# Performance work log

Measured on AMD Instinct MI355X. Metric: run time of the kernel, lower is better.

## Reference

```python
import jax, jax.numpy as jnp
import numpy as np


def _conv1x1(x, w, b=None):
    # x: [B, Cin, N, S], w: [Cout, Cin], 1x1 Conv2d
    y = jnp.einsum('oc,bcns->bons', w, x)
    if b is not None:
        y = y + b[None, :, None, None]
    return y


def setup_inputs() -> dict:
    key = jax.random.key(0)
    ks = jax.random.split(key, 16)
    B, Cin, N, K = 4, 128, 16384, 16
    MID, OUT, SHARE, PT = 64, 128, 8, 10
    s = 0.05
    inp = {
        'sm_feats': jax.random.normal(ks[0], (B, Cin, N, K), jnp.float32),
        'sm_ppfs': jax.random.normal(ks[1], (B, PT, N, K), jnp.float32),
        'conv0_w': jax.random.normal(ks[2], (OUT, Cin), jnp.float32) * s,
        'conv0_b': jax.random.normal(ks[3], (OUT,), jnp.float32) * s,
        'conv1_w': jax.random.normal(ks[4], (MID, OUT), jnp.float32) * s,
        'conv1_b': jax.random.normal(ks[5], (MID,), jnp.float32) * s,
        'conv2_w': jax.random.normal(ks[6], (MID, OUT), jnp.float32) * s,
        'conv2_b': jax.random.normal(ks[7], (MID,), jnp.float32) * s,
        'conv3_w': jax.random.normal(ks[8], (MID, OUT), jnp.float32) * s,
        'conv3_b': jax.random.normal(ks[9], (MID,), jnp.float32) * s,
        'convw1_w': jax.random.normal(ks[10], (MID // SHARE, MID * K), jnp.float32) * s,
        'convw2_w': jax.random.normal(ks[11], (K * MID // SHARE, MID // SHARE), jnp.float32) * s,
        'convw2_b': jax.random.normal(ks[12], (K * MID // SHARE,), jnp.float32) * s,
        'convout_w': jax.random.normal(ks[13], (OUT, MID), jnp.float32) * s,
        'convout_b': jax.random.normal(ks[14], (OUT,), jnp.float32) * s,
        'pt1_w': jax.random.normal(ks[15], (MID, PT), jnp.float32) * s,
        'pt2_w': jax.random.normal(jax.random.fold_in(key, 99), (MID, MID), jnp.float32) * s,
    }
    return inp


def reference(sm_feats, sm_ppfs, conv0_w, conv0_b, conv1_w, conv1_b, conv2_w, conv2_b,
              conv3_w, conv3_b, convw1_w, convw2_w, convw2_b, convout_w, convout_b,
              pt1_w, pt2_w):
    xn = jax.nn.relu(_conv1x1(sm_feats, conv0_w, conv0_b))  # [B, OUT, N, K]
    x = xn[..., :1]                                          # center point feature
    identity = x
    x1 = _conv1x1(x, conv1_w, conv1_b)       # [B, MID, N, 1]
    x2 = _conv1x1(xn, conv2_w, conv2_b)      # [B, MID, N, K]
    x3 = _conv1x1(xn, conv3_w, conv3_b)      # [B, MID, N, K]
    ptf = _conv1x1(jax.nn.relu(_conv1x1(sm_ppfs, pt1_w)), pt2_w)  # [B, MID, N, K]
    x3 = x3 + ptf
    xfs = x1 - x2 + ptf                      # [B, MID, N, K]
    B, MID, N, K = xfs.shape
    share = MID // convw1_w.shape[0]
    xfs = jnp.transpose(xfs, (0, 1, 3, 2)).reshape(B, MID * K, 1, N)
    h = jax.nn.relu(_conv1x1(xfs, convw1_w))            # [B, MID//share, 1, N]
    w = _conv1x1(h, convw2_w, convw2_b)                  # [B, K*MID//share, 1, N]
    w = jax.nn.softmax(w.reshape(B, MID // share, K, N), axis=2)
    w = jnp.transpose(w, (0, 1, 3, 2))                   # [B, MID//share, N, K]
    w = jnp.tile(w, (1, share, 1, 1))                    # [B, MID, N, K]
    out = jax.nn.relu(jnp.sum(w * x3, axis=3, keepdims=True))  # [B, MID, N, 1]
    out = (_conv1x1(out, convout_w, convout_b) + identity).squeeze(3)  # [B, OUT, N]
    return out
```

## Files before the change

kernel.cpp:

```cpp
#include <hip/hip_runtime.h>
#include <hip/hip_bf16.h>


typedef __attribute__((ext_vector_type(8))) short bf16x8;
typedef __attribute__((ext_vector_type(4))) float f32x4;
typedef __attribute__((ext_vector_type(4))) unsigned short us4;

#define MFMA(a, b, c) __builtin_amdgcn_mfma_f32_16x16x32_bf16((a), (b), (c), 0, 0, 0)

#define OFF_F    0
#define OFF_X2   0
#define OFF_PTF  17408
#define OFF_XN   34816
#define OFF_X3   34816
#define OFF_XFS  52224
#define OFF_P    69632
#define OFF_WS   69632
#define OFF_HP   73984
#define OFF_HB   76032
#define OFF_OM   76288
#define OFF_X1   77824
#define OFF_XC   78848
#define SMEM_BYTES 80896

#define WS_W0  0
#define WS_W1  16384
#define WS_W2  24576
#define WS_W3  32768
#define WS_P1  40960
#define WS_P2  43008
#define WS_CW1 47104
#define WS_WO  63488
#define WS_TOTAL 71680

__device__ __forceinline__ unsigned short f2b(float f) {
    union { __hip_bfloat16 h; unsigned short u; } v;
    v.h = __float2bfloat16(f);
    return v.u;
}
__device__ __forceinline__ float b2f(unsigned short u) {
    union { unsigned u; float f; } v;
    v.u = ((unsigned)u) << 16;
    return v.f;
}
__device__ __forceinline__ us4 pk4(float a, float b, float c, float d) {
    us4 r; r[0] = f2b(a); r[1] = f2b(b); r[2] = f2b(c); r[3] = f2b(d); return r;
}
__device__ __forceinline__ bf16x8 ldb(const unsigned short* p) {
    return *(const bf16x8*)p;
}

__global__ __launch_bounds__(512, 1)
void convert_weights(const float* __restrict__ w0, const float* __restrict__ w1,
                     const float* __restrict__ w2, const float* __restrict__ w3,
                     const float* __restrict__ p1, const float* __restrict__ p2,
                     const float* __restrict__ cw1, const float* __restrict__ wo,
                     unsigned short* __restrict__ ws) {
    int i = blockIdx.x * 512 + threadIdx.x;
    if (i >= WS_TOTAL) return;
    float v;
    if (i < 16384)      v = w0[i];
    else if (i < 24576) v = w1[i - 16384];
    else if (i < 32768) v = w2[i - 24576];
    else if (i < 40960) v = w3[i - 32768];
    else if (i < 43008) { int r = i - 40960, row = r >> 5, k = r & 31;
                          v = (k < 10) ? p1[row * 10 + k] : 0.f; }
    else if (i < 47104) v = p2[i - 43008];
    else if (i < 63488) { int r = i - 47104, j = r >> 10, kc = r & 1023;
                          v = (j < 8) ? cw1[j * 1024 + (kc & 63) * 16 + (kc >> 6)] : 0.f; }
    else                v = wo[i - 63488];
    ws[i] = f2b(v);
}

__global__ __launch_bounds__(512, 4)
void fused_model_kernel(const float* __restrict__ feats, const float* __restrict__ ppfs,
                        const unsigned short* __restrict__ wsb,
                        const float* __restrict__ b0, const float* __restrict__ b1,
                        const float* __restrict__ b2, const float* __restrict__ b3,
                        const float* __restrict__ cw2, const float* __restrict__ cb2,
                        const float* __restrict__ bo, float* __restrict__ out) {
    extern __shared__ char smem[];
    const int tid = threadIdx.x;
    const int W = tid >> 6;
    const int lane = tid & 63;
    const int kk = lane & 15;
    const int g = lane >> 4;
    const int bid = blockIdx.x;
    const int b = bid >> 11;
    const int n0 = (bid & 2047) * 8;

    {
        const int kq = tid & 3, ci = tid >> 2;
        #pragma unroll
        for (int pos = 0; pos < 8; ++pos) {
            f32x4 v = *(const f32x4*)(feats + (((size_t)b * 128 + ci) * 16384 + (n0 + pos)) * 16 + kq * 4);
            char* base = smem + OFF_F + pos * 4352 + ci * 2;
            *(unsigned short*)(base + (kq * 4 + 0) * 272) = f2b(v[0]);
            *(unsigned short*)(base + (kq * 4 + 1) * 272) = f2b(v[1]);
            *(unsigned short*)(base + (kq * 4 + 2) * 272) = f2b(v[2]);
            *(unsigned short*)(base + (kq * 4 + 3) * 272) = f2b(v[3]);
        }
        if (tid < 320) {
            int pos = tid / 40, r = tid % 40, p = r >> 2, kq2 = r & 3;
            f32x4 v = *(const f32x4*)(ppfs + (((size_t)b * 10 + p) * 16384 + (n0 + pos)) * 16 + kq2 * 4);
            char* base = smem + OFF_P + pos * 1024 + p * 2;
            *(unsigned short*)(base + (kq2 * 4 + 0) * 64) = f2b(v[0]);
            *(unsigned short*)(base + (kq2 * 4 + 1) * 64) = f2b(v[1]);
            *(unsigned short*)(base + (kq2 * 4 + 2) * 64) = f2b(v[2]);
            *(unsigned short*)(base + (kq2 * 4 + 3) * 64) = f2b(v[3]);
        } else {
            for (int z = tid - 320; z < 1408; z += 192) {
                int pos = z / 176, rr = z % 176, ks = rr / 11, dw = rr % 11;
                *(unsigned*)(smem + OFF_P + pos * 1024 + ks * 64 + 20 + dw * 4) = 0u;
            }
        }
    }
    __syncthreads();

    {
        bf16x8 a0[4];
        #pragma unroll
        for (int kt = 0; kt < 4; ++kt) a0[kt] = ldb(wsb + WS_W0 + (16 * W + kk) * 128 + kt * 32 + 8 * g);
        f32x4 bv = *(const f32x4*)(b0 + 16 * W + 4 * g);
        #pragma unroll
        for (int pos = 0; pos < 8; ++pos) {
            f32x4 acc = {0.f, 0.f, 0.f, 0.f};
            #pragma unroll
            for (int kt = 0; kt < 4; ++kt) {
                bf16x8 bf = *(const bf16x8*)(smem + OFF_F + pos * 4352 + kk * 272 + (kt * 32 + 8 * g) * 2);
                acc = MFMA(a0[kt], bf, acc);
            }
            us4 xw = pk4(fmaxf(acc[0] + bv[0], 0.f), fmaxf(acc[1] + bv[1], 0.f),
                         fmaxf(acc[2] + bv[2], 0.f), fmaxf(acc[3] + bv[3], 0.f));
            *(us4*)(smem + OFF_XN + pos * 4352 + kk * 272 + (16 * W + 4 * g) * 2) = xw;
            if (kk == 0) *(us4*)(smem + OFF_XC + pos * 256 + (16 * W + 4 * g) * 2) = xw;
        }
    }
    __syncthreads();

    if (W < 4) {
        bf16x8 a1[4], a2[4][2];
        #pragma unroll
        for (int mt = 0; mt < 4; ++mt) {
            a1[mt] = ldb(wsb + WS_P1 + (16 * mt + kk) * 32 + 8 * g);
            a2[mt][0] = ldb(wsb + WS_P2 + (16 * mt + kk) * 64 + 8 * g);
            a2[mt][1] = ldb(wsb + WS_P2 + (16 * mt + kk) * 64 + 32 + 8 * g);
        }
        const int sel = g >> 1;
        const int sa = kk + 16 * ((2 * g) & 3);
        const int sb = kk + 16 * ((2 * g + 1) & 3);
        #pragma unroll
        for (int pp = 0; pp < 2; ++pp) {
            const int pos = 2 * W + pp;
            bf16x8 bp = *(const bf16x8*)(smem + OFF_P + pos * 1024 + kk * 64 + 16 * g);
            int pkd[4][2];
            #pragma unroll
            for (int mt = 0; mt < 4; ++mt) {
                f32x4 hv = {0.f, 0.f, 0.f, 0.f};
                hv = MFMA(a1[mt], bp, hv);
                us4 t = pk4(fmaxf(hv[0], 0.f), fmaxf(hv[1], 0.f),
                            fmaxf(hv[2], 0.f), fmaxf(hv[3], 0.f));
                pkd[mt][0] = ((int*)&t)[0];
                pkd[mt][1] = ((int*)&t)[1];
            }
            union { int d[4]; bf16x8 v; } bh0, bh1;
            bh0.d[0] = sel ? __shfl(pkd[1][0], sa, 64) : __shfl(pkd[0][0], sa, 64);
            bh0.d[1] = sel ? __shfl(pkd[1][1], sa, 64) : __shfl(pkd[0][1], sa, 64);
            bh0.d[2] = sel ? __shfl(pkd[1][0], sb, 64) : __shfl(pkd[0][0], sb, 64);
            bh0.d[3] = sel ? __shfl(pkd[1][1], sb, 64) : __shfl(pkd[0][1], sb, 64);
            bh1.d[0] = sel ? __shfl(pkd[3][0], sa, 64) : __shfl(pkd[2][0], sa, 64);
            bh1.d[1] = sel ? __shfl(pkd[3][1], sa, 64) : __shfl(pkd[2][1], sa, 64);
            bh1.d[2] = sel ? __shfl(pkd[3][0], sb, 64) : __shfl(pkd[2][0], sb, 64);
            bh1.d[3] = sel ? __shfl(pkd[3][1], sb, 64) : __shfl(pkd[2][1], sb, 64);
            #pragma unroll
            for (int mt = 0; mt < 4; ++mt) {
                f32x4 acc = {0.f, 0.f, 0.f, 0.f};
                acc = MFMA(a2[mt][0], bh0.v, acc);
                acc = MFMA(a2[mt][1], bh1.v, acc);
                *(us4*)(smem + OFF_PTF + pos * 2176 + kk * 136 + (16 * mt + 4 * g) * 2) =
                    pk4(acc[0], acc[1], acc[2], acc[3]);
            }
        }
    } else {
        const int mt = W - 4;
        bf16x8 aw2[4], aw1[4];
        #pragma unroll
        for (int kt = 0; kt < 4; ++kt) {
            aw2[kt] = ldb(wsb + WS_W2 + (16 * mt + kk) * 128 + kt * 32 + 8 * g);
            aw1[kt] = ldb(wsb + WS_W1 + (16 * mt + kk) * 128 + kt * 32 + 8 * g);
        }
        f32x4 b2v = *(const f32x4*)(b2 + 16 * mt + 4 * g);
        #pragma unroll
        for (int pos = 0; pos < 8; ++pos) {
            f32x4 acc = {0.f, 0.f, 0.f, 0.f};
            #pragma unroll
            for (int kt = 0; kt < 4; ++kt) {
                bf16x8 bf = *(const bf16x8*)(smem + OFF_XN + pos * 4352 + kk * 272 + (kt * 32 + 8 * g) * 2);
                acc = MFMA(aw2[kt], bf, acc);
            }
            *(us4*)(smem + OFF_X2 + pos * 2176 + kk * 136 + (16 * mt + 4 * g) * 2) =
                pk4(acc[0] + b2v[0], acc[1] + b2v[1], acc[2] + b2v[2], acc[3] + b2v[3]);
        }
        f32x4 a1c = {0.f, 0.f, 0.f, 0.f};
        #pragma unroll
        for (int kt = 0; kt < 4; ++kt) {
            bf16x8 bf = *(const bf16x8*)(smem + OFF_XN + (kk & 7) * 4352 + (kt * 32 + 8 * g) * 2);
            a1c = MFMA(aw1[kt], bf, a1c);
        }
        if (kk < 8) {
            f32x4 b1v = *(const f32x4*)(b1 + 16 * mt + 4 * g);
            *(us4*)(smem + OFF_X1 + kk * 128 + (16 * mt + 4 * g) * 2) =
                pk4(a1c[0] + b1v[0], a1c[1] + b1v[1], a1c[2] + b1v[2], a1c[3] + b1v[3]);
        }
    }
    __syncthreads();

    f32x4 acc3[4];
    {
        const int mt = W & 3, ph = W >> 2;
        bf16x8 aw3[4];
        #pragma unroll
        for (int kt = 0; kt < 4; ++kt)
            aw3[kt] = ldb(wsb + WS_W3 + (16 * mt + kk) * 128 + kt * 32 + 8 * g);
        #pragma unroll
        for (int pp = 0; pp < 4; ++pp) {
            const int pos = ph * 4 + pp;
            f32x4 acc = {0.f, 0.f, 0.f, 0.f};
            #pragma unroll
            for (int kt = 0; kt < 4; ++kt) {
                bf16x8 bf = *(const bf16x8*)(smem + OFF_XN + pos * 4352 + kk * 272 + (kt * 32 + 8 * g) * 2);
                acc = MFMA(aw3[kt], bf, acc);
            }
            acc3[pp] = acc;
        }
    }
    __syncthreads();

    {
        const int mt = W & 3, ph = W >> 2;
        f32x4 b3v = *(const f32x4*)(b3 + 16 * mt + 4 * g);
        #pragma unroll
        for (int pp = 0; pp < 4; ++pp) {
            const int pos = ph * 4 + pp;
            us4 ptfv = *(const us4*)(smem + OFF_PTF + pos * 2176 + kk * 136 + (16 * mt + 4 * g) * 2);
            us4 x2v  = *(const us4*)(smem + OFF_X2  + pos * 2176 + kk * 136 + (16 * mt + 4 * g) * 2);
            us4 x1v  = *(const us4*)(smem + OFF_X1  + pos * 128 + (16 * mt + 4 * g) * 2);
            float pf0 = b2f(ptfv[0]), pf1 = b2f(ptfv[1]), pf2 = b2f(ptfv[2]), pf3 = b2f(ptfv[3]);
            *(us4*)(smem + OFF_X3 + pos * 2176 + kk * 136 + (16 * mt + 4 * g) * 2) =
                pk4(acc3[pp][0] + b3v[0] + pf0, acc3[pp][1] + b3v[1] + pf1,
                    acc3[pp][2] + b3v[2] + pf2, acc3[pp][3] + b3v[3] + pf3);
            *(us4*)(smem + OFF_XFS + pos * 2080 + (kk * 64 + 16 * mt + 4 * g) * 2) =
                pk4(b2f(x1v[0]) - b2f(x2v[0]) + pf0, b2f(x1v[1]) - b2f(x2v[1]) + pf1,
                    b2f(x1v[2]) - b2f(x2v[2]) + pf2, b2f(x1v[3]) - b2f(x2v[3]) + pf3);
        }
    }
    __syncthreads();

    {
        bf16x8 acw[4];
        #pragma unroll
        for (int kt = 0; kt < 4; ++kt)
            acw[kt] = ldb(wsb + WS_CW1 + kk * 1024 + W * 128 + kt * 32 + 8 * g);
        f32x4 acc = {0.f, 0.f, 0.f, 0.f};
        #pragma unroll
        for (int kt = 0; kt < 4; ++kt) {
            bf16x8 bf = *(const bf16x8*)(smem + OFF_XFS + (kk & 7) * 2080 + (W * 128 + kt * 32 + 8 * g) * 2);
            acc = MFMA(acw[kt], bf, acc);
        }
        if (kk < 8 && g < 2) {
            #pragma unroll
            for (int r = 0; r < 4; ++r)
                *(float*)(smem + OFF_HP + W * 256 + ((4 * g + r) * 8 + kk) * 4) = acc[r];
        }
    }
    __syncthreads();
    if (tid < 64) {
        float s = 0.f;
        #pragma unroll
        for (int w = 0; w < 8; ++w) s += *(const float*)(smem + OFF_HP + w * 256 + tid * 4);
        *(float*)(smem + OFF_HB + tid * 4) = fmaxf(s, 0.f);
    }
    __syncthreads();

    {
        #pragma unroll
        for (int pp = 0; pp < 2; ++pp) {
            const int item = tid + 512 * pp;
            const int pos = item >> 7, c = item & 127, k = c & 15, j2 = c >> 4;
            float wl = cb2[c];
            f32x4 w20 = *(const f32x4*)(cw2 + c * 8);
            f32x4 w21 = *(const f32x4*)(cw2 + c * 8 + 4);
            #pragma unroll
            for (int j = 0; j < 4; ++j) {
                wl += w20[j] * *(const float*)(smem + OFF_HB + (j * 8 + pos) * 4);
                wl += w21[j] * *(const float*)(smem + OFF_HB + ((j + 4) * 8 + pos) * 4);
            }
            float mx = wl;
            for (int off = 8; off; off >>= 1) mx = fmaxf(mx, __shfl_xor(mx, off, 16));
            float e = __expf(wl - mx);
            float ss = e;
            for (int off = 8; off; off >>= 1) ss += __shfl_xor(ss, off, 16);
            *(float*)(smem + OFF_WS + pos * 544 + j2 * 68 + k * 4) = e / ss;
        }
    }
    __syncthreads();

    {
        const int pos = W, m = lane, j2 = m & 7;
        const char* wsp = smem + OFF_WS + pos * 544 + j2 * 68;
        const char* x3b = smem + OFF_X3 + pos * 2176 + m * 2;
        float s = 0.f;
        #pragma unroll
        for (int k = 0; k < 16; ++k)
            s += *(const float*)(wsp + k * 4) * b2f(*(const unsigned short*)(x3b + k * 136));
        *(unsigned short*)(smem + OFF_OM + pos * 144 + m * 2) = f2b(fmaxf(s, 0.f));
    }
    __syncthreads();

    {
        f32x4 acc = {0.f, 0.f, 0.f, 0.f};
        #pragma unroll
        for (int kt = 0; kt < 2; ++kt) {
            bf16x8 bf = *(const bf16x8*)(smem + OFF_OM + (kk & 7) * 144 + (kt * 32 + 8 * g) * 2);
            acc = MFMA(ldb(wsb + WS_WO + (16 * W + kk) * 64 + kt * 32 + 8 * g), bf, acc);
        }
        if (kk < 8) {
            f32x4 bv = *(const f32x4*)(bo + 16 * W + 4 * g);
            #pragma unroll
            for (int r = 0; r < 4; ++r) {
                int o = 16 * W + 4 * g + r;
                out[((size_t)b * 128 + o) * 16384 + n0 + kk] =
                    acc[r] + bv[r] + b2f(*(const unsigned short*)(smem + OFF_XC + kk * 256 + o * 2));
            }
        }
    }
}

extern "C" void kernel_launch(void* const* d_in, const int* in_sizes, int n_in,
                              void* d_out, int out_size, void* d_ws, size_t ws_size,
                              hipStream_t stream) {
    (void)in_sizes; (void)n_in; (void)out_size; (void)ws_size;
    const float* feats = (const float*)d_in[0];
    const float* ppfs  = (const float*)d_in[1];
    const float* w0  = (const float*)d_in[2];
    const float* b0  = (const float*)d_in[3];
    const float* w1  = (const float*)d_in[4];
    const float* b1  = (const float*)d_in[5];
    const float* w2  = (const float*)d_in[6];
    const float* b2  = (const float*)d_in[7];
    const float* w3  = (const float*)d_in[8];
    const float* b3  = (const float*)d_in[9];
    const float* cw1 = (const float*)d_in[10];
    const float* cw2 = (const float*)d_in[11];
    const float* cb2 = (const float*)d_in[12];
    const float* wo  = (const float*)d_in[13];
    const float* bo  = (const float*)d_in[14];
    const float* p1  = (const float*)d_in[15];
    const float* p2  = (const float*)d_in[16];
    float* out = (float*)d_out;
    unsigned short* wsb = (unsigned short*)d_ws;

    convert_weights<<<dim3((WS_TOTAL + 511) / 512), dim3(512), 0, stream>>>(
        w0, w1, w2, w3, p1, p2, cw1, wo, wsb);

    (void)hipFuncSetAttribute(reinterpret_cast<const void*>(fused_model_kernel),
                              hipFuncAttributeMaxDynamicSharedMemorySize, SMEM_BYTES);
    fused_model_kernel<<<dim3(8192), dim3(512), SMEM_BYTES, stream>>>(
        feats, ppfs, wsb, b0, b1, b2, b3, cw2, cb2, bo, out);
}
```

Baseline: 330.8 us.

## Rebalance stages across waves, swizzle LDS layouts, and drop block barriers

Every wave now computes the ptf path for one position, and the x2 and x3 convolutions are fused so they share the xn B-fragments. The stage boundaries are reorganised so that several __syncthreads are removed. The convw1 reduction becomes a per-wave dot product with shuffle reductions, which removes the partial-sum buffer and two block barriers, and softmax and the weighted sum run per wave behind wave barriers. The feats and xfs LDS layouts are XOR-swizzled or rotated to cut bank conflicts, and x1 is computed from a compact center-feature buffer. The trade-off is more scalar FMA work in the convw1 stage and more weights reloaded per wave from global memory.

```diff
diff --git a/kernel.cpp b/kernel.cpp
--- a/kernel.cpp
+++ b/kernel.cpp
@@ -16,12 +16,11 @@
 #define OFF_XFS  52224
 #define OFF_P    69632
 #define OFF_WS   69632
-#define OFF_HP   73984
-#define OFF_HB   76032
-#define OFF_OM   76288
+#define OFF_HB   73984
+#define OFF_OM   74240
 #define OFF_X1   77824
-#define OFF_XC   78848
-#define SMEM_BYTES 80896
+#define OFF_XC   78912
+#define SMEM_BYTES 81088
 
 #define WS_W0  0
 #define WS_W1  16384
@@ -91,10 +90,11 @@
 
     {
         const int kq = tid & 3, ci = tid >> 2;
+        const int cisw = (ci * 2) ^ (kq << 4);
         #pragma unroll
         for (int pos = 0; pos < 8; ++pos) {
             f32x4 v = *(const f32x4*)(feats + (((size_t)b * 128 + ci) * 16384 + (n0 + pos)) * 16 + kq * 4);
-            char* base = smem + OFF_F + pos * 4352 + ci * 2;
+            char* base = smem + OFF_F + pos * 4352 + cisw;
             *(unsigned short*)(base + (kq * 4 + 0) * 272) = f2b(v[0]);
             *(unsigned short*)(base + (kq * 4 + 1) * 272) = f2b(v[1]);
             *(unsigned short*)(base + (kq * 4 + 2) * 272) = f2b(v[2]);
@@ -122,134 +122,116 @@
         #pragma unroll
         for (int kt = 0; kt < 4; ++kt) a0[kt] = ldb(wsb + WS_W0 + (16 * W + kk) * 128 + kt * 32 + 8 * g);
         f32x4 bv = *(const f32x4*)(b0 + 16 * W + 4 * g);
+        const int fsw = ((kk >> 2) & 3) << 4;
         #pragma unroll
         for (int pos = 0; pos < 8; ++pos) {
             f32x4 acc = {0.f, 0.f, 0.f, 0.f};
             #pragma unroll
             for (int kt = 0; kt < 4; ++kt) {
-                bf16x8 bf = *(const bf16x8*)(smem + OFF_F + pos * 4352 + kk * 272 + (kt * 32 + 8 * g) * 2);
+                bf16x8 bf = *(const bf16x8*)(smem + OFF_F + pos * 4352 + kk * 272 + ((kt * 64 + 16 * g) ^ fsw));
                 acc = MFMA(a0[kt], bf, acc);
             }
             us4 xw = pk4(fmaxf(acc[0] + bv[0], 0.f), fmaxf(acc[1] + bv[1], 0.f),
                          fmaxf(acc[2] + bv[2], 0.f), fmaxf(acc[3] + bv[3], 0.f));
             *(us4*)(smem + OFF_XN + pos * 4352 + kk * 272 + (16 * W + 4 * g) * 2) = xw;
-            if (kk == 0) *(us4*)(smem + OFF_XC + pos * 256 + (16 * W + 4 * g) * 2) = xw;
-        }
-    }
-    __syncthreads();
-
-    if (W < 4) {
-        bf16x8 a1[4], a2[4][2];
-        #pragma unroll
-        for (int mt = 0; mt < 4; ++mt) {
-            a1[mt] = ldb(wsb + WS_P1 + (16 * mt + kk) * 32 + 8 * g);
-            a2[mt][0] = ldb(wsb + WS_P2 + (16 * mt + kk) * 64 + 8 * g);
-            a2[mt][1] = ldb(wsb + WS_P2 + (16 * mt + kk) * 64 + 32 + 8 * g);
+            if (kk == 0) *(us4*)(smem + OFF_XC + pos * 272 + (16 * W + 4 * g) * 2) = xw;
+        }
+    }
+    __syncthreads();
+
+    f32x4 acc3[4];
+    {
+        const int pos = W;
+        bf16x8 bp = *(const bf16x8*)(smem + OFF_P + pos * 1024 + kk * 64 + 16 * g);
+        int pkd[4][2];
+        #pragma unroll
+        for (int mtx = 0; mtx < 4; ++mtx) {
+            bf16x8 a1 = ldb(wsb + WS_P1 + (16 * mtx + kk) * 32 + 8 * g);
+            f32x4 hv = {0.f, 0.f, 0.f, 0.f};
+            hv = MFMA(a1, bp, hv);
+            us4 t = pk4(fmaxf(hv[0], 0.f), fmaxf(hv[1], 0.f), fmaxf(hv[2], 0.f), fmaxf(hv[3], 0.f));
+            pkd[mtx][0] = ((int*)&t)[0];
+            pkd[mtx][1] = ((int*)&t)[1];
         }
         const int sel = g >> 1;
         const int sa = kk + 16 * ((2 * g) & 3);
         const int sb = kk + 16 * ((2 * g + 1) & 3);
-        #pragma unroll
-        for (int pp = 0; pp < 2; ++pp) {
-            const int pos = 2 * W + pp;
-            bf16x8 bp = *(const bf16x8*)(smem + OFF_P + pos * 1024 + kk * 64 + 16 * g);
-            int pkd[4][2];
-            #pragma unroll
-            for (int mt = 0; mt < 4; ++mt) {
-                f32x4 hv = {0.f, 0.f, 0.f, 0.f};
-                hv = MFMA(a1[mt], bp, hv);
-                us4 t = pk4(fmaxf(hv[0], 0.f), fmaxf(hv[1], 0.f),
-                            fmaxf(hv[2], 0.f), fmaxf(hv[3], 0.f));
-                pkd[mt][0] = ((int*)&t)[0];
-                pkd[mt][1] = ((int*)&t)[1];
-            }
-            union { int d[4]; bf16x8 v; } bh0, bh1;
-            bh0.d[0] = sel ? __shfl(pkd[1][0], sa, 64) : __shfl(pkd[0][0], sa, 64);
-            bh0.d[1] = sel ? __shfl(pkd[1][1], sa, 64) : __shfl(pkd[0][1], sa, 64);
-            bh0.d[2] = sel ? __shfl(pkd[1][0], sb, 64) : __shfl(pkd[0][0], sb, 64);
-            bh0.d[3] = sel ? __shfl(pkd[1][1], sb, 64) : __shfl(pkd[0][1], sb, 64);
-            bh1.d[0] = sel ? __shfl(pkd[3][0], sa, 64) : __shfl(pkd[2][0], sa, 64);
-            bh1.d[1] = sel ? __shfl(pkd[3][1], sa, 64) : __shfl(pkd[2][1], sa, 64);
-            bh1.d[2] = sel ? __shfl(pkd[3][0], sb, 64) : __shfl(pkd[2][0], sb, 64);
-            bh1.d[3] = sel ? __shfl(pkd[3][1], sb, 64) : __shfl(pkd[2][1], sb, 64);
-            #pragma unroll
-            for (int mt = 0; mt < 4; ++mt) {
-                f32x4 acc = {0.f, 0.f, 0.f, 0.f};
-                acc = MFMA(a2[mt][0], bh0.v, acc);
-                acc = MFMA(a2[mt][1], bh1.v, acc);
-                *(us4*)(smem + OFF_PTF + pos * 2176 + kk * 136 + (16 * mt + 4 * g) * 2) =
-                    pk4(acc[0], acc[1], acc[2], acc[3]);
-            }
-        }
-    } else {
-        const int mt = W - 4;
-        bf16x8 aw2[4], aw1[4];
+        union { int d[4]; bf16x8 v; } bh0, bh1;
+        bh0.d[0] = sel ? __shfl(pkd[1][0], sa, 64) : __shfl(pkd[0][0], sa, 64);
+        bh0.d[1] = sel ? __shfl(pkd[1][1], sa, 64) : __shfl(pkd[0][1], sa, 64);
+        bh0.d[2] = sel ? __shfl(pkd[1][0], sb, 64) : __shfl(pkd[0][0], sb, 64);
+        bh0.d[3] = sel ? __shfl(pkd[1][1], sb, 64) : __shfl(pkd[0][1], sb, 64);
+        bh1.d[0] = sel ? __shfl(pkd[3][0], sa, 64) : __shfl(pkd[2][0], sa, 64);
+        bh1.d[1] = sel ? __shfl(pkd[3][1], sa, 64) : __shfl(pkd[2][1], sa, 64);
+        bh1.d[2] = sel ? __shfl(pkd[3][0], sb, 64) : __shfl(pkd[2][0], sb, 64);
+        bh1.d[3] = sel ? __shfl(pkd[3][1], sb, 64) : __shfl(pkd[2][1], sb, 64);
+        #pragma unroll
+        for (int mtx = 0; mtx < 4; ++mtx) {
+            f32x4 a = {0.f, 0.f, 0.f, 0.f};
+            a = MFMA(ldb(wsb + WS_P2 + (16 * mtx + kk) * 64 + 8 * g), bh0.v, a);
+            a = MFMA(ldb(wsb + WS_P2 + (16 * mtx + kk) * 64 + 32 + 8 * g), bh1.v, a);
+            *(us4*)(smem + OFF_PTF + pos * 2176 + kk * 136 + (16 * mtx + 4 * g) * 2) =
+                pk4(a[0], a[1], a[2], a[3]);
+        }
+    }
+    {
+        const int mt = W & 3, posh = W >> 2;
+        bf16x8 aw2[4], aw3[4];
         #pragma unroll
         for (int kt = 0; kt < 4; ++kt) {
             aw2[kt] = ldb(wsb + WS_W2 + (16 * mt + kk) * 128 + kt * 32 + 8 * g);
-            aw1[kt] = ldb(wsb + WS_W1 + (16 * mt + kk) * 128 + kt * 32 + 8 * g);
+            aw3[kt] = ldb(wsb + WS_W3 + (16 * mt + kk) * 128 + kt * 32 + 8 * g);
         }
         f32x4 b2v = *(const f32x4*)(b2 + 16 * mt + 4 * g);
         #pragma unroll
-        for (int pos = 0; pos < 8; ++pos) {
-            f32x4 acc = {0.f, 0.f, 0.f, 0.f};
+        for (int pp = 0; pp < 4; ++pp) {
+            const int pos = posh * 4 + pp;
+            bf16x8 bx[4];
+            #pragma unroll
+            for (int kt = 0; kt < 4; ++kt)
+                bx[kt] = *(const bf16x8*)(smem + OFF_XN + pos * 4352 + kk * 272 + (kt * 64 + 16 * g));
+            f32x4 a = {0.f, 0.f, 0.f, 0.f};
+            f32x4 c = {0.f, 0.f, 0.f, 0.f};
             #pragma unroll
             for (int kt = 0; kt < 4; ++kt) {
-                bf16x8 bf = *(const bf16x8*)(smem + OFF_XN + pos * 4352 + kk * 272 + (kt * 32 + 8 * g) * 2);
-                acc = MFMA(aw2[kt], bf, acc);
+                a = MFMA(aw2[kt], bx[kt], a);
+                c = MFMA(aw3[kt], bx[kt], c);
             }
             *(us4*)(smem + OFF_X2 + pos * 2176 + kk * 136 + (16 * mt + 4 * g) * 2) =
-                pk4(acc[0] + b2v[0], acc[1] + b2v[1], acc[2] + b2v[2], acc[3] + b2v[3]);
-        }
-        f32x4 a1c = {0.f, 0.f, 0.f, 0.f};
-        #pragma unroll
-        for (int kt = 0; kt < 4; ++kt) {
-            bf16x8 bf = *(const bf16x8*)(smem + OFF_XN + (kk & 7) * 4352 + (kt * 32 + 8 * g) * 2);
-            a1c = MFMA(aw1[kt], bf, a1c);
-        }
-        if (kk < 8) {
-            f32x4 b1v = *(const f32x4*)(b1 + 16 * mt + 4 * g);
-            *(us4*)(smem + OFF_X1 + kk * 128 + (16 * mt + 4 * g) * 2) =
-                pk4(a1c[0] + b1v[0], a1c[1] + b1v[1], a1c[2] + b1v[2], a1c[3] + b1v[3]);
-        }
-    }
-    __syncthreads();
-
-    f32x4 acc3[4];
-    {
-        const int mt = W & 3, ph = W >> 2;
-        bf16x8 aw3[4];
-        #pragma unroll
-        for (int kt = 0; kt < 4; ++kt)
-            aw3[kt] = ldb(wsb + WS_W3 + (16 * mt + kk) * 128 + kt * 32 + 8 * g);
+                pk4(a[0] + b2v[0], a[1] + b2v[1], a[2] + b2v[2], a[3] + b2v[3]);
+            acc3[pp] = c;
+        }
+        if (W < 4) {
+            f32x4 a = {0.f, 0.f, 0.f, 0.f};
+            #pragma unroll
+            for (int kt = 0; kt < 4; ++kt) {
+                bf16x8 bf = *(const bf16x8*)(smem + OFF_XC + (kk & 7) * 272 + (kt * 64 + 16 * g));
+                a = MFMA(ldb(wsb + WS_W1 + (16 * W + kk) * 128 + kt * 32 + 8 * g), bf, a);
+            }
+            if (kk < 8) {
+                f32x4 b1v = *(const f32x4*)(b1 + 16 * W + 4 * g);
+                *(us4*)(smem + OFF_X1 + kk * 136 + (16 * W + 4 * g) * 2) =
+                    pk4(a[0] + b1v[0], a[1] + b1v[1], a[2] + b1v[2], a[3] + b1v[3]);
+            }
+        }
+    }
+    __syncthreads();
+
+    {
+        const int mt = W & 3, posh = W >> 2;
+        f32x4 b3v = *(const f32x4*)(b3 + 16 * mt + 4 * g);
+        const int rot = (32 * mt + 8 * g + 16 * kk) & 127;
         #pragma unroll
         for (int pp = 0; pp < 4; ++pp) {
-            const int pos = ph * 4 + pp;
-            f32x4 acc = {0.f, 0.f, 0.f, 0.f};
-            #pragma unroll
-            for (int kt = 0; kt < 4; ++kt) {
-                bf16x8 bf = *(const bf16x8*)(smem + OFF_XN + pos * 4352 + kk * 272 + (kt * 32 + 8 * g) * 2);
-                acc = MFMA(aw3[kt], bf, acc);
-            }
-            acc3[pp] = acc;
-        }
-    }
-    __syncthreads();
-
-    {
-        const int mt = W & 3, ph = W >> 2;
-        f32x4 b3v = *(const f32x4*)(b3 + 16 * mt + 4 * g);
-        #pragma unroll
-        for (int pp = 0; pp < 4; ++pp) {
-            const int pos = ph * 4 + pp;
+            const int pos = posh * 4 + pp;
             us4 ptfv = *(const us4*)(smem + OFF_PTF + pos * 2176 + kk * 136 + (16 * mt + 4 * g) * 2);
             us4 x2v  = *(const us4*)(smem + OFF_X2  + pos * 2176 + kk * 136 + (16 * mt + 4 * g) * 2);
-            us4 x1v  = *(const us4*)(smem + OFF_X1  + pos * 128 + (16 * mt + 4 * g) * 2);
+            us4 x1v  = *(const us4*)(smem + OFF_X1  + pos * 136 + (16 * mt + 4 * g) * 2);
             float pf0 = b2f(ptfv[0]), pf1 = b2f(ptfv[1]), pf2 = b2f(ptfv[2]), pf3 = b2f(ptfv[3]);
             *(us4*)(smem + OFF_X3 + pos * 2176 + kk * 136 + (16 * mt + 4 * g) * 2) =
                 pk4(acc3[pp][0] + b3v[0] + pf0, acc3[pp][1] + b3v[1] + pf1,
                     acc3[pp][2] + b3v[2] + pf2, acc3[pp][3] + b3v[3] + pf3);
-            *(us4*)(smem + OFF_XFS + pos * 2080 + (kk * 64 + 16 * mt + 4 * g) * 2) =
+            *(us4*)(smem + OFF_XFS + pos * 2048 + kk * 128 + rot) =
                 pk4(b2f(x1v[0]) - b2f(x2v[0]) + pf0, b2f(x1v[1]) - b2f(x2v[1]) + pf1,
                     b2f(x1v[2]) - b2f(x2v[2]) + pf2, b2f(x1v[3]) - b2f(x2v[3]) + pf3);
         }
@@ -257,63 +239,58 @@
     __syncthreads();
 
     {
-        bf16x8 acw[4];
-        #pragma unroll
-        for (int kt = 0; kt < 4; ++kt)
-            acw[kt] = ldb(wsb + WS_CW1 + kk * 1024 + W * 128 + kt * 32 + 8 * g);
-        f32x4 acc = {0.f, 0.f, 0.f, 0.f};
-        #pragma unroll
-        for (int kt = 0; kt < 4; ++kt) {
-            bf16x8 bf = *(const bf16x8*)(smem + OFF_XFS + (kk & 7) * 2080 + (W * 128 + kt * 32 + 8 * g) * 2);
-            acc = MFMA(acw[kt], bf, acc);
-        }
-        if (kk < 8 && g < 2) {
-            #pragma unroll
-            for (int r = 0; r < 4; ++r)
-                *(float*)(smem + OFF_HP + W * 256 + ((4 * g + r) * 8 + kk) * 4) = acc[r];
-        }
-    }
-    __syncthreads();
-    if (tid < 64) {
+        const int j = lane >> 3, c8 = lane & 7;
+        const unsigned short* wrow = wsb + WS_CW1 + j * 1024 + c8 * 128;
+        const char* xbase = smem + OFF_XFS + W * 2048;
         float s = 0.f;
         #pragma unroll
-        for (int w = 0; w < 8; ++w) s += *(const float*)(smem + OFF_HP + w * 256 + tid * 4);
-        *(float*)(smem + OFF_HB + tid * 4) = fmaxf(s, 0.f);
-    }
-    __syncthreads();
-
-    {
-        #pragma unroll
-        for (int pp = 0; pp < 2; ++pp) {
-            const int item = tid + 512 * pp;
-            const int pos = item >> 7, c = item & 127, k = c & 15, j2 = c >> 4;
+        for (int u = 0; u < 16; ++u) {
+            const int k = 2 * c8 + (u >> 3);
+            const int byt = ((u & 7) * 16 + 16 * k) & 127;
+            bf16x8 xv = *(const bf16x8*)(xbase + k * 128 + byt);
+            bf16x8 wv = ldb(wrow + u * 8);
+            #pragma unroll
+            for (int i = 0; i < 8; ++i)
+                s += b2f((unsigned short)xv[i]) * b2f((unsigned short)wv[i]);
+        }
+        s += __shfl_xor(s, 1);
+        s += __shfl_xor(s, 2);
+        s += __shfl_xor(s, 4);
+        if (c8 == 0) *(float*)(smem + OFF_HB + (j * 8 + W) * 4) = fmaxf(s, 0.f);
+        __builtin_amdgcn_wave_barrier();
+        __builtin_amdgcn_sched_barrier(0);
+
+        float hbv[8];
+        #pragma unroll
+        for (int jj = 0; jj < 8; ++jj) hbv[jj] = *(const float*)(smem + OFF_HB + (jj * 8 + W) * 4);
+        #pragma unroll
+        for (int it = 0; it < 2; ++it) {
+            const int c = it * 64 + lane;
             float wl = cb2[c];
             f32x4 w20 = *(const f32x4*)(cw2 + c * 8);
             f32x4 w21 = *(const f32x4*)(cw2 + c * 8 + 4);
             #pragma unroll
-            for (int j = 0; j < 4; ++j) {
-                wl += w20[j] * *(const float*)(smem + OFF_HB + (j * 8 + pos) * 4);
-                wl += w21[j] * *(const float*)(smem + OFF_HB + ((j + 4) * 8 + pos) * 4);
+            for (int jj = 0; jj < 4; ++jj) {
+                wl += w20[jj] * hbv[jj];
+                wl += w21[jj] * hbv[4 + jj];
             }
             float mx = wl;
             for (int off = 8; off; off >>= 1) mx = fmaxf(mx, __shfl_xor(mx, off, 16));
             float e = __expf(wl - mx);
             float ss = e;
             for (int off = 8; off; off >>= 1) ss += __shfl_xor(ss, off, 16);
-            *(float*)(smem + OFF_WS + pos * 544 + j2 * 68 + k * 4) = e / ss;
-        }
-    }
-    __syncthreads();
-
-    {
-        const int pos = W, m = lane, j2 = m & 7;
-        const char* wsp = smem + OFF_WS + pos * 544 + j2 * 68;
-        const char* x3b = smem + OFF_X3 + pos * 2176 + m * 2;
-        float s = 0.f;
+            *(float*)(smem + OFF_WS + W * 544 + (4 * it + g) * 68 + kk * 4) = e / ss;
+        }
+        __builtin_amdgcn_wave_barrier();
+        __builtin_amdgcn_sched_barrier(0);
+
+        const float* wsp = (const float*)(smem + OFF_WS + W * 544 + (lane & 7) * 68);
+        const char* x3b = smem + OFF_X3 + W * 2176 + lane * 2;
+        float so = 0.f;
         #pragma unroll
         for (int k = 0; k < 16; ++k)
-            s += *(const float*)(wsp + k * 4) * b2f(*(const unsigned short*)(x3b + k * 136));
-        *(unsigned short*)(smem + OFF_OM + pos * 144 + m * 2) = f2b(fmaxf(s, 0.f));
+            so += wsp[k] * b2f(*(const unsigned short*)(x3b + k * 136));
+        *(unsigned short*)(smem + OFF_OM + W * 144 + lane * 2) = f2b(fmaxf(so, 0.f));
     }
     __syncthreads();
 
@@ -321,7 +298,7 @@
         f32x4 acc = {0.f, 0.f, 0.f, 0.f};
         #pragma unroll
         for (int kt = 0; kt < 2; ++kt) {
-            bf16x8 bf = *(const bf16x8*)(smem + OFF_OM + (kk & 7) * 144 + (kt * 32 + 8 * g) * 2);
+            bf16x8 bf = *(const bf16x8*)(smem + OFF_OM + (kk & 7) * 144 + (kt * 64 + 16 * g));
             acc = MFMA(ldb(wsb + WS_WO + (16 * W + kk) * 64 + kt * 32 + 8 * g), bf, acc);
         }
         if (kk < 8) {
@@ -330,7 +307,7 @@
             for (int r = 0; r < 4; ++r) {
                 int o = 16 * W + 4 * g + r;
                 out[((size_t)b * 128 + o) * 16384 + n0 + kk] =
-                    acc[r] + bv[r] + b2f(*(const unsigned short*)(smem + OFF_XC + kk * 256 + o * 2));
+                    acc[r] + bv[r] + b2f(*(const unsigned short*)(smem + OFF_XC + kk * 272 + o * 2));
             }
         }
     }
```

Result: slower. 432.7 us (+30.8%).
